# Performance work log

Hardware: AMD Instinct MI355X
Metric: run time of the kernel (lower is better)

## Reference

```python
import jax, jax.numpy as jnp
import numpy as np

S = 16          # slice count (init kwarg)
EPS = 1e-5      # BN2d default eps


def markov_sub(m, s):
    """Vectorized get_markov_sub. m: [C, C] -> [s, C, C].
    ms[i][a,b] = where(m[i,b] > 0, m[a,b], 0); mss[k] = max over rows i in slice k.
    Equivalent closed form via per-column any/all positivity of the slice rows."""
    C = m.shape[0]
    pos = (m > 0.0).reshape(s, C // s, C)          # [s, slice_size, C]
    any_p = pos.any(axis=1)[:, None, :]            # [s, 1, C]
    all_p = pos.all(axis=1)[:, None, :]            # [s, 1, C]
    mb = m[None, :, :]                             # [1, C, C]
    return jnp.where(all_p, mb,
                     jnp.where(any_p, jnp.maximum(mb, 0.0), jnp.zeros_like(mb)))


def setup_inputs() -> dict:
    key = jax.random.key(0)
    ks = jax.random.split(key, 8)
    N, C, H, W = 4, 256, 32, 32
    s = S
    feats = jax.random.normal(ks[0], (N, C, H, W), jnp.float32)
    adj_matrix = jax.random.normal(ks[1], (N, C, C), jnp.float32)
    # three 1x1 conv layers: in = S*C, out = C (stacked on leading axis)
    conv_w = jax.random.normal(ks[2], (3, C, s * C), jnp.float32) / np.sqrt(s * C).astype(np.float32)
    conv_b = jax.random.normal(ks[3], (3, C), jnp.float32) * 0.01
    bn_gamma = jnp.ones((3, C), jnp.float32)
    bn_beta = jnp.zeros((3, C), jnp.float32)
    bn_mean = jax.random.normal(ks[4], (3, C), jnp.float32) * 0.1
    bn_var = jax.random.uniform(ks[5], (3, C), jnp.float32, minval=0.5, maxval=1.5)
    return {"feats": feats, "adj_matrix": adj_matrix, "conv_w": conv_w,
            "conv_b": conv_b, "bn_gamma": bn_gamma, "bn_beta": bn_beta,
            "bn_mean": bn_mean, "bn_var": bn_var}


def reference(feats, adj_matrix, conv_w, conv_b, bn_gamma, bn_beta, bn_mean, bn_var):
    N, C, H, W = feats.shape
    s = S
    # per-sample markov sub-adjacencies, computed once and reused across layers
    mss = jax.vmap(lambda m: markov_sub(m, s))(adj_matrix)      # [N, S, C, C]
    mss = mss.reshape(N, s * C, C)                              # [N, S*C, C]
    outs = []
    x = feats
    for l in range(3):
        xp = x.reshape(N, C, H * W)                             # [N, C, HW]
        y = jnp.einsum('nkc,ncp->nkp', mss, xp)                 # sparse.mm -> [N, S*C, HW]
        y = jnp.einsum('ok,nkp->nop', conv_w[l], y) + conv_b[l][None, :, None]
        scale = (bn_gamma[l] * jax.lax.rsqrt(bn_var[l] + EPS))[None, :, None]
        y = (y - bn_mean[l][None, :, None]) * scale + bn_beta[l][None, :, None]
        y = jax.nn.relu(y).reshape(N, C, H, W)
        outs.append(y)
        x = y
    return tuple(outs)
```

## Files before the change

kernel.cpp:

```cpp
#include <hip/hip_runtime.h>
#include <stdint.h>

#define CC   256
#define NB   4
#define HWP  1024
#define EPSV 1e-5f

typedef __attribute__((ext_vector_type(8))) short bf16x8;
typedef __attribute__((ext_vector_type(4))) float f32x4;

__device__ __forceinline__ ushort f2bf(float f) {
    uint32_t u = __float_as_uint(f);
    uint32_t r = (u + 0x7FFFu + ((u >> 16) & 1u)) >> 16;
    return (ushort)r;
}

__global__ __launch_bounds__(256) void mplusT_flags(const float* __restrict__ adj,
                                                    ushort* __restrict__ mpT,
                                                    unsigned int* __restrict__ count,
                                                    unsigned int* __restrict__ badlist) {
    const int n = blockIdx.y;
    const int at = blockIdx.x >> 2, bt = blockIdx.x & 3;
    const int a0 = at * 64, b0 = bt * 64;
    const float* m = adj + (size_t)n * CC * CC;
    __shared__ float Ms[64][68];
    const int t = threadIdx.x;
    {
        const int ar = t >> 2, bq = (t & 3) * 16;
        const float* src = m + (size_t)(a0 + ar) * CC + b0 + bq;
#pragma unroll
        for (int i = 0; i < 4; ++i)
            *(float4*)&Ms[ar][bq + i * 4] = *(const float4*)(src + i * 4);
    }
    __syncthreads();
    {
        const int bl = t >> 2, ac = (t & 3) * 16;
        ushort* dst = mpT + ((size_t)n * CC + b0 + bl) * CC + a0 + ac;
#pragma unroll
        for (int a4 = 0; a4 < 4; ++a4) {
            ushort4 o;
            o.x = f2bf(fmaxf(Ms[ac + a4 * 4 + 0][bl], 0.f));
            o.y = f2bf(fmaxf(Ms[ac + a4 * 4 + 1][bl], 0.f));
            o.z = f2bf(fmaxf(Ms[ac + a4 * 4 + 2][bl], 0.f));
            o.w = f2bf(fmaxf(Ms[ac + a4 * 4 + 3][bl], 0.f));
            *(ushort4*)(dst + a4 * 4) = o;
        }
    }
    {
        const int kl = t >> 6, bl = t & 63;
        bool allp = true, anyp = false;
#pragma unroll
        for (int i = 0; i < 16; ++i) {
            bool p = Ms[kl * 16 + i][bl] > 0.0f;
            allp = allp && p;
            anyp = anyp || p;
        }
        const int f = allp ? 2 : (anyp ? 1 : 0);
        if (f != 1) {
            unsigned int pos = atomicAdd(count, 1u);
            const int k = at * 4 + kl;
            badlist[pos] = (unsigned int)((f << 16) | (n << 12) | (k << 8) | (b0 + bl));
        }
    }
}

__global__ __launch_bounds__(256) void cwsum_kernel(const float* __restrict__ w,
                                                    ushort* __restrict__ cwS) {
    const int idx = (blockIdx.x * 256 + threadIdx.x) * 4;
    const int l = idx >> 16;
    const int o = (idx >> 8) & 255;
    const int a = idx & 255;
    const float* src = w + (size_t)l * 1048576 + (size_t)o * 4096 + a;
    float4 s = {0.f, 0.f, 0.f, 0.f};
#pragma unroll
    for (int k = 0; k < 16; ++k) {
        float4 v = *(const float4*)(src + k * 256);
        s.x += v.x; s.y += v.y; s.z += v.z; s.w += v.w;
    }
    ushort4 ob = {f2bf(s.x), f2bf(s.y), f2bf(s.z), f2bf(s.w)};
    *(ushort4*)(cwS + idx) = ob;
}

__global__ __launch_bounds__(256) void correction_kernel(const float* __restrict__ adj,
                                                         const float* __restrict__ conv_w,
                                                         const unsigned int* __restrict__ count,
                                                         const unsigned int* __restrict__ badlist,
                                                         float* __restrict__ Wdelta) {
    const int l = blockIdx.y;
    const unsigned int cnt = *count;
    __shared__ float v[256];
    const int t = threadIdx.x;
    for (unsigned int i = blockIdx.x; i < cnt; i += gridDim.x) {
        const unsigned int e = badlist[i];
        const int b = e & 255, k = (e >> 8) & 15, n = (e >> 12) & 3, f = (e >> 16) & 3;
        __syncthreads();
        const float mv = adj[(size_t)n * 65536 + (size_t)t * CC + b];
        v[t] = (f == 0) ? fmaxf(mv, 0.f) : fmaxf(-mv, 0.f);
        __syncthreads();
        const float* cw = conv_w + (size_t)l * 1048576 + (size_t)t * 4096 + k * 256;
        float s = 0.f;
#pragma unroll 8
        for (int a = 0; a < 256; ++a) s += cw[a] * v[a];
        atomicAdd(Wdelta + (((size_t)(l * 4 + n) * 256 + t) * 256 + b), -s);
    }
}

__global__ __launch_bounds__(256) void wbase_mfma(const ushort* __restrict__ cwS,
                                                  const ushort* __restrict__ mpT,
                                                  const float* __restrict__ gamma,
                                                  const float* __restrict__ var,
                                                  const unsigned int* __restrict__ count,
                                                  const float* __restrict__ Wdelta,
                                                  ushort* __restrict__ Ws) {
    const int tile = blockIdx.x;
    const int ln = blockIdx.y;
    const int l = ln >> 2, n = ln & 3;
    const int trow = (tile >> 2) * 64, tcol = (tile & 3) * 64;
    const ushort* A = cwS + (size_t)l * 65536;
    const ushort* B = mpT + (size_t)n * 65536;
    __shared__ ushort Al[64][40];
    __shared__ ushort Bl[64][40];
    const int t = threadIdx.x;
    const int wv = t >> 6, L = t & 63;
    const int wr = (wv >> 1) * 32, wc = (wv & 1) * 32;
    const int l16 = L & 15, q = L >> 4;
    const int r0 = t >> 2, kq0 = (t & 3) * 8;
    f32x4 acc[2][2];
#pragma unroll
    for (int i = 0; i < 2; ++i)
#pragma unroll
        for (int j = 0; j < 2; ++j)
            acc[i][j] = (f32x4){0.f, 0.f, 0.f, 0.f};

    for (int kt = 0; kt < 8; ++kt) {
        const int kk = kt * 32;
        int4 av = *(const int4*)(A + (size_t)(trow + r0) * CC + kk + kq0);
        int4 bv = *(const int4*)(B + (size_t)(tcol + r0) * CC + kk + kq0);
        __syncthreads();
        *(int4*)&Al[r0][kq0] = av;
        *(int4*)&Bl[r0][kq0] = bv;
        __syncthreads();
        bf16x8 af[2], bfr[2];
#pragma unroll
        for (int i = 0; i < 2; ++i)
            af[i] = *(const bf16x8*)&Al[wr + i * 16 + l16][q * 8];
#pragma unroll
        for (int j = 0; j < 2; ++j)
            bfr[j] = *(const bf16x8*)&Bl[wc + j * 16 + l16][q * 8];
#pragma unroll
        for (int i = 0; i < 2; ++i)
#pragma unroll
            for (int j = 0; j < 2; ++j)
                acc[i][j] = __builtin_amdgcn_mfma_f32_16x16x32_bf16(af[i], bfr[j], acc[i][j], 0, 0, 0);
    }

    const unsigned int cnt = *count;
    ushort* W = Ws + (size_t)ln * 65536;
    const float* Wd = Wdelta + (size_t)ln * 65536;
#pragma unroll
    for (int i = 0; i < 2; ++i)
#pragma unroll
        for (int j = 0; j < 2; ++j) {
            const int ob = trow + wr + i * 16 + q * 4;
            const int b  = tcol + wc + j * 16 + l16;
#pragma unroll
            for (int r = 0; r < 4; ++r) {
                const int o = ob + r;
                float a = acc[i][j][r];
                if (cnt) a += Wd[(size_t)o * CC + b];
                const float sc = gamma[l * CC + o] * rsqrtf(var[l * CC + o] + EPSV);
                W[(size_t)o * CC + b] = f2bf(a * sc);
            }
        }
}

__global__ __launch_bounds__(256) void fused_layers(const float* __restrict__ feats,
                                                    const ushort* __restrict__ Ws,
                                                    const float* __restrict__ conv_b,
                                                    const float* __restrict__ gamma,
                                                    const float* __restrict__ beta,
                                                    const float* __restrict__ mean,
                                                    const float* __restrict__ var,
                                                    float* __restrict__ out) {
    const int n = blockIdx.y;
    const int p0 = blockIdx.x * 16;
    __shared__ ushort xl[2][16][264];
    const int t = threadIdx.x;
    const int wv = t >> 6, L = t & 63;
    const int l16 = L & 15, q = L >> 4;

    {
        const float* src = feats + ((size_t)n * CC + t) * HWP + p0;
        float v[16];
#pragma unroll
        for (int i = 0; i < 4; ++i)
            *(float4*)&v[i * 4] = *(const float4*)(src + i * 4);
#pragma unroll
        for (int i = 0; i < 16; ++i)
            xl[0][i][t] = f2bf(v[i]);
    }
    __syncthreads();

    int cur = 0;
    for (int l = 0; l < 3; ++l) {
        const ushort* Bw = Ws + (size_t)(l * 4 + n) * 65536;
        f32x4 acc[4];
#pragma unroll
        for (int jj = 0; jj < 4; ++jj) acc[jj] = (f32x4){0.f, 0.f, 0.f, 0.f};

#pragma unroll
        for (int kt = 0; kt < 8; ++kt) {
            const int kk = kt * 32;
            bf16x8 af = *(const bf16x8*)&xl[cur][l16][kk + q * 8];
#pragma unroll
            for (int jj = 0; jj < 4; ++jj) {
                const int o = (wv * 4 + jj) * 16 + l16;
                bf16x8 bv = *(const bf16x8*)(Bw + (size_t)o * CC + kk + q * 8);
                acc[jj] = __builtin_amdgcn_mfma_f32_16x16x32_bf16(af, bv, acc[jj], 0, 0, 0);
            }
        }

        float* outn = out + (size_t)(l * 4 + n) * CC * HWP;
#pragma unroll
        for (int jj = 0; jj < 4; ++jj) {
            const int o = (wv * 4 + jj) * 16 + l16;
            const float sc = gamma[l * CC + o] * rsqrtf(var[l * CC + o] + EPSV);
            const float b2 = sc * (conv_b[l * CC + o] - mean[l * CC + o]) + beta[l * CC + o];
            const float v0 = fmaxf(acc[jj][0] + b2, 0.f);
            const float v1 = fmaxf(acc[jj][1] + b2, 0.f);
            const float v2 = fmaxf(acc[jj][2] + b2, 0.f);
            const float v3 = fmaxf(acc[jj][3] + b2, 0.f);
            *(float4*)(outn + (size_t)o * HWP + p0 + q * 4) = (float4){v0, v1, v2, v3};
            if (l < 2) {
                xl[cur ^ 1][q * 4 + 0][o] = f2bf(v0);
                xl[cur ^ 1][q * 4 + 1][o] = f2bf(v1);
                xl[cur ^ 1][q * 4 + 2][o] = f2bf(v2);
                xl[cur ^ 1][q * 4 + 3][o] = f2bf(v3);
            }
        }
        __syncthreads();
        cur ^= 1;
    }
}

extern "C" void kernel_launch(void* const* d_in, const int* in_sizes, int n_in,
                              void* d_out, int out_size, void* d_ws, size_t ws_size,
                              hipStream_t stream) {
    const float* feats  = (const float*)d_in[0];
    const float* adj    = (const float*)d_in[1];
    const float* conv_w = (const float*)d_in[2];
    const float* conv_b = (const float*)d_in[3];
    const float* gamma  = (const float*)d_in[4];
    const float* beta   = (const float*)d_in[5];
    const float* mean   = (const float*)d_in[6];
    const float* var    = (const float*)d_in[7];
    float* out = (float*)d_out;

    char* ws = (char*)d_ws;
    float*        Wdelta  = (float*)ws;
    unsigned int* count   = (unsigned int*)(ws + 3145728);
    unsigned int* badlist = (unsigned int*)(ws + 3145792);
    ushort*       cwS     = (ushort*)(ws + 3211328);
    ushort*       mpT     = (ushort*)(ws + 3604544);
    ushort*       Wsb     = (ushort*)(ws + 4128832);

    hipMemsetAsync(ws, 0, 3145792, stream);

    mplusT_flags<<<dim3(16, NB), 256, 0, stream>>>(adj, mpT, count, badlist);
    cwsum_kernel<<<192, 256, 0, stream>>>(conv_w, cwS);
    correction_kernel<<<dim3(48, 3), 256, 0, stream>>>(adj, conv_w, count, badlist, Wdelta);
    wbase_mfma<<<dim3(16, 12), 256, 0, stream>>>(cwS, mpT, gamma, var, count, Wdelta, Wsb);
    fused_layers<<<dim3(64, NB), 256, 0, stream>>>(feats, Wsb, conv_b, gamma, beta, mean, var, out);
}
```

Before: 129.6 us.

## Merge prep kernels and fold sparse correction into the MFMA epilogue

Combines the adjacency transpose/flag pass and the conv-weight slice sum into one prep kernel. The per-(n,b,k) any/all flags are now stored as a byte array instead of an atomic badlist. The correction kernel, the Wdelta buffer and its memset are removed; the weight-build MFMA kernel checks the flags per column and computes the rare correction dot products inline. This cuts two launches and a 3 MB memset, but a column with non-uniform flags costs a serial scalar 256-long loop in the epilogue. With random inputs such columns should be very rare.

```diff
diff --git a/kernel.cpp b/kernel.cpp
--- a/kernel.cpp
+++ b/kernel.cpp
@@ -15,102 +15,73 @@
     return (ushort)r;
 }
 
-__global__ __launch_bounds__(256) void mplusT_flags(const float* __restrict__ adj,
-                                                    ushort* __restrict__ mpT,
-                                                    unsigned int* __restrict__ count,
-                                                    unsigned int* __restrict__ badlist) {
-    const int n = blockIdx.y;
-    const int at = blockIdx.x >> 2, bt = blockIdx.x & 3;
-    const int a0 = at * 64, b0 = bt * 64;
-    const float* m = adj + (size_t)n * CC * CC;
-    __shared__ float Ms[64][68];
+__global__ __launch_bounds__(256) void prep_kernel(const float* __restrict__ adj,
+                                                   const float* __restrict__ conv_w,
+                                                   ushort* __restrict__ mpT,
+                                                   uint8_t* __restrict__ flags,
+                                                   ushort* __restrict__ cwS) {
     const int t = threadIdx.x;
-    {
-        const int ar = t >> 2, bq = (t & 3) * 16;
-        const float* src = m + (size_t)(a0 + ar) * CC + b0 + bq;
-#pragma unroll
-        for (int i = 0; i < 4; ++i)
-            *(float4*)&Ms[ar][bq + i * 4] = *(const float4*)(src + i * 4);
-    }
-    __syncthreads();
-    {
-        const int bl = t >> 2, ac = (t & 3) * 16;
-        ushort* dst = mpT + ((size_t)n * CC + b0 + bl) * CC + a0 + ac;
-#pragma unroll
-        for (int a4 = 0; a4 < 4; ++a4) {
-            ushort4 o;
-            o.x = f2bf(fmaxf(Ms[ac + a4 * 4 + 0][bl], 0.f));
-            o.y = f2bf(fmaxf(Ms[ac + a4 * 4 + 1][bl], 0.f));
-            o.z = f2bf(fmaxf(Ms[ac + a4 * 4 + 2][bl], 0.f));
-            o.w = f2bf(fmaxf(Ms[ac + a4 * 4 + 3][bl], 0.f));
-            *(ushort4*)(dst + a4 * 4) = o;
-        }
-    }
-    {
-        const int kl = t >> 6, bl = t & 63;
-        bool allp = true, anyp = false;
-#pragma unroll
-        for (int i = 0; i < 16; ++i) {
-            bool p = Ms[kl * 16 + i][bl] > 0.0f;
-            allp = allp && p;
-            anyp = anyp || p;
-        }
-        const int f = allp ? 2 : (anyp ? 1 : 0);
-        if (f != 1) {
-            unsigned int pos = atomicAdd(count, 1u);
-            const int k = at * 4 + kl;
-            badlist[pos] = (unsigned int)((f << 16) | (n << 12) | (k << 8) | (b0 + bl));
-        }
-    }
-}
-
-__global__ __launch_bounds__(256) void cwsum_kernel(const float* __restrict__ w,
-                                                    ushort* __restrict__ cwS) {
-    const int idx = (blockIdx.x * 256 + threadIdx.x) * 4;
-    const int l = idx >> 16;
-    const int o = (idx >> 8) & 255;
-    const int a = idx & 255;
-    const float* src = w + (size_t)l * 1048576 + (size_t)o * 4096 + a;
-    float4 s = {0.f, 0.f, 0.f, 0.f};
-#pragma unroll
-    for (int k = 0; k < 16; ++k) {
-        float4 v = *(const float4*)(src + k * 256);
-        s.x += v.x; s.y += v.y; s.z += v.z; s.w += v.w;
-    }
-    ushort4 ob = {f2bf(s.x), f2bf(s.y), f2bf(s.z), f2bf(s.w)};
-    *(ushort4*)(cwS + idx) = ob;
-}
-
-__global__ __launch_bounds__(256) void correction_kernel(const float* __restrict__ adj,
-                                                         const float* __restrict__ conv_w,
-                                                         const unsigned int* __restrict__ count,
-                                                         const unsigned int* __restrict__ badlist,
-                                                         float* __restrict__ Wdelta) {
-    const int l = blockIdx.y;
-    const unsigned int cnt = *count;
-    __shared__ float v[256];
-    const int t = threadIdx.x;
-    for (unsigned int i = blockIdx.x; i < cnt; i += gridDim.x) {
-        const unsigned int e = badlist[i];
-        const int b = e & 255, k = (e >> 8) & 15, n = (e >> 12) & 3, f = (e >> 16) & 3;
-        __syncthreads();
-        const float mv = adj[(size_t)n * 65536 + (size_t)t * CC + b];
-        v[t] = (f == 0) ? fmaxf(mv, 0.f) : fmaxf(-mv, 0.f);
-        __syncthreads();
-        const float* cw = conv_w + (size_t)l * 1048576 + (size_t)t * 4096 + k * 256;
-        float s = 0.f;
-#pragma unroll 8
-        for (int a = 0; a < 256; ++a) s += cw[a] * v[a];
-        atomicAdd(Wdelta + (((size_t)(l * 4 + n) * 256 + t) * 256 + b), -s);
+    if (blockIdx.x < 64) {
+        const int bb = blockIdx.x;
+        const int n = bb >> 4;
+        const int at = (bb >> 2) & 3, bt = bb & 3;
+        const int a0 = at * 64, b0 = bt * 64;
+        const float* m = adj + (size_t)n * CC * CC;
+        __shared__ float Ms[64][68];
+        {
+            const int ar = t >> 2, bq = (t & 3) * 16;
+            const float* src = m + (size_t)(a0 + ar) * CC + b0 + bq;
+#pragma unroll
+            for (int i = 0; i < 4; ++i)
+                *(float4*)&Ms[ar][bq + i * 4] = *(const float4*)(src + i * 4);
+        }
+        __syncthreads();
+        {
+            const int bl = t >> 2, ac = (t & 3) * 16;
+            ushort* dst = mpT + ((size_t)n * CC + b0 + bl) * CC + a0 + ac;
+#pragma unroll
+            for (int a4 = 0; a4 < 4; ++a4) {
+                ushort4 o;
+                o.x = f2bf(fmaxf(Ms[ac + a4 * 4 + 0][bl], 0.f));
+                o.y = f2bf(fmaxf(Ms[ac + a4 * 4 + 1][bl], 0.f));
+                o.z = f2bf(fmaxf(Ms[ac + a4 * 4 + 2][bl], 0.f));
+                o.w = f2bf(fmaxf(Ms[ac + a4 * 4 + 3][bl], 0.f));
+                *(ushort4*)(dst + a4 * 4) = o;
+            }
+        }
+        {
+            const int kl = t >> 6, bl = t & 63;
+            bool allp = true, anyp = false;
+#pragma unroll
+            for (int i = 0; i < 16; ++i) {
+                bool p = Ms[kl * 16 + i][bl] > 0.0f;
+                allp = allp && p;
+                anyp = anyp || p;
+            }
+            const uint8_t f = allp ? (uint8_t)2 : (anyp ? (uint8_t)1 : (uint8_t)0);
+            flags[(((size_t)n * CC) + b0 + bl) * 16 + at * 4 + kl] = f;
+        }
+    } else {
+        const int idx = ((blockIdx.x - 64) * 256 + t) * 4;
+        const float* src = conv_w + ((size_t)(idx >> 8)) * 4096 + (idx & 255);
+        float4 s = {0.f, 0.f, 0.f, 0.f};
+#pragma unroll
+        for (int k = 0; k < 16; ++k) {
+            float4 v = *(const float4*)(src + k * 256);
+            s.x += v.x; s.y += v.y; s.z += v.z; s.w += v.w;
+        }
+        ushort4 ob = {f2bf(s.x), f2bf(s.y), f2bf(s.z), f2bf(s.w)};
+        *(ushort4*)(cwS + idx) = ob;
     }
 }
 
 __global__ __launch_bounds__(256) void wbase_mfma(const ushort* __restrict__ cwS,
                                                   const ushort* __restrict__ mpT,
+                                                  const uint8_t* __restrict__ flags,
+                                                  const float* __restrict__ adj,
+                                                  const float* __restrict__ conv_w,
                                                   const float* __restrict__ gamma,
                                                   const float* __restrict__ var,
-                                                  const unsigned int* __restrict__ count,
-                                                  const float* __restrict__ Wdelta,
                                                   ushort* __restrict__ Ws) {
     const int tile = blockIdx.x;
     const int ln = blockIdx.y;
@@ -154,24 +125,44 @@
                 acc[i][j] = __builtin_amdgcn_mfma_f32_16x16x32_bf16(af[i], bfr[j], acc[i][j], 0, 0, 0);
     }
 
-    const unsigned int cnt = *count;
     ushort* W = Ws + (size_t)ln * 65536;
-    const float* Wd = Wdelta + (size_t)ln * 65536;
-#pragma unroll
-    for (int i = 0; i < 2; ++i)
-#pragma unroll
-        for (int j = 0; j < 2; ++j) {
+#pragma unroll
+    for (int j = 0; j < 2; ++j) {
+        const int b = tcol + wc + j * 16 + l16;
+        const uint8_t* fb = flags + (((size_t)n * CC) + b) * 16;
+        const uint4 fv = *(const uint4*)fb;
+        const bool bad = (fv.x != 0x01010101u) || (fv.y != 0x01010101u) ||
+                         (fv.z != 0x01010101u) || (fv.w != 0x01010101u);
+        if (bad) {
+            for (int k = 0; k < 16; ++k) {
+                const int f = fb[k];
+                if (f == 1) continue;
+                for (int i = 0; i < 2; ++i) {
+                    for (int r = 0; r < 4; ++r) {
+                        const int o = trow + wr + i * 16 + q * 4 + r;
+                        const float* cw = conv_w + (size_t)l * 1048576 + (size_t)o * 4096 + k * 256;
+                        float s = 0.f;
+                        for (int a = 0; a < 256; ++a) {
+                            const float mv = adj[(size_t)n * 65536 + (size_t)a * CC + b];
+                            const float vv = (f == 0) ? fmaxf(mv, 0.f) : fmaxf(-mv, 0.f);
+                            s += cw[a] * vv;
+                        }
+                        acc[i][j][r] -= s;
+                    }
+                }
+            }
+        }
+#pragma unroll
+        for (int i = 0; i < 2; ++i) {
             const int ob = trow + wr + i * 16 + q * 4;
-            const int b  = tcol + wc + j * 16 + l16;
 #pragma unroll
             for (int r = 0; r < 4; ++r) {
                 const int o = ob + r;
-                float a = acc[i][j][r];
-                if (cnt) a += Wd[(size_t)o * CC + b];
                 const float sc = gamma[l * CC + o] * rsqrtf(var[l * CC + o] + EPSV);
-                W[(size_t)o * CC + b] = f2bf(a * sc);
-            }
-        }
+                W[(size_t)o * CC + b] = f2bf(acc[i][j][r] * sc);
+            }
+        }
+    }
 }
 
 __global__ __launch_bounds__(256) void fused_layers(const float* __restrict__ feats,
@@ -257,18 +248,12 @@
     float* out = (float*)d_out;
 
     char* ws = (char*)d_ws;
-    float*        Wdelta  = (float*)ws;
-    unsigned int* count   = (unsigned int*)(ws + 3145728);
-    unsigned int* badlist = (unsigned int*)(ws + 3145792);
-    ushort*       cwS     = (ushort*)(ws + 3211328);
-    ushort*       mpT     = (ushort*)(ws + 3604544);
-    ushort*       Wsb     = (ushort*)(ws + 4128832);
-
-    hipMemsetAsync(ws, 0, 3145792, stream);
-
-    mplusT_flags<<<dim3(16, NB), 256, 0, stream>>>(adj, mpT, count, badlist);
-    cwsum_kernel<<<192, 256, 0, stream>>>(conv_w, cwS);
-    correction_kernel<<<dim3(48, 3), 256, 0, stream>>>(adj, conv_w, count, badlist, Wdelta);
-    wbase_mfma<<<dim3(16, 12), 256, 0, stream>>>(cwS, mpT, gamma, var, count, Wdelta, Wsb);
+    uint8_t* flags = (uint8_t*)ws;
+    ushort*  cwS   = (ushort*)(ws + 16384);
+    ushort*  mpT   = (ushort*)(ws + 409600);
+    ushort*  Wsb   = (ushort*)(ws + 933888);
+
+    prep_kernel<<<256, 256, 0, stream>>>(adj, conv_w, mpT, flags, cwS);
+    wbase_mfma<<<dim3(16, 12), 256, 0, stream>>>(cwS, mpT, flags, adj, conv_w, gamma, var, Wsb);
     fused_layers<<<dim3(64, NB), 256, 0, stream>>>(feats, Wsb, conv_b, gamma, beta, mean, var, out);
 }
```

Result: slower. 196.7 us (+51.7%).
